# Kernel tuning notes

Measured on AMD Instinct MI355X. Metric: run time of the kernel, lower is better.

Reference implementation:

```python
import jax, jax.numpy as jnp
import numpy as np

B, L, D, K, H = 2, 384, 1024, 128, 32
NUM_EDGES = 25600
NUM_T = 1000
SCALING = K ** -0.5
SQRT_2PI = float(np.sqrt(2.0 * np.pi))


def setup_inputs() -> dict:
    key = jax.random.key(0)
    ks = jax.random.split(key, 20)
    s = 0.02
    inp = {}
    inp["token_id"] = jax.random.randint(ks[0], (B, L), 0, 160)
    inp["is_periodic"] = jnp.zeros((B,), dtype=bool)
    inp["pos"] = 5.0 * jax.random.normal(ks[1], (B, L, 3), dtype=jnp.float32)
    inp["adj"] = jnp.ones((B, L, L), dtype=bool)
    inp["node_type_edge"] = jax.random.randint(ks[2], (B, L, L, 2), 0, NUM_EDGES)
    inp["time_step"] = jax.random.uniform(ks[3], (B, L), dtype=jnp.float32)
    inp["clean_mask"] = jnp.zeros((B, L), dtype=bool)
    # parameters
    inp["embed_w"] = s * jax.random.normal(ks[4], (160, D), dtype=jnp.float32)
    inp["Wpos"] = s * jax.random.normal(ks[5], (K, 3), dtype=jnp.float32)
    inp["Wpfe"] = s * jax.random.normal(ks[6], (D, K), dtype=jnp.float32)
    inp["gbf_means"] = jax.random.normal(ks[7], (K,), dtype=jnp.float32)
    inp["gbf_stds"] = 0.5 + jax.random.uniform(ks[8], (K,), dtype=jnp.float32)
    inp["gbf_mul"] = 1.0 + s * jax.random.normal(ks[9], (NUM_EDGES, 1), dtype=jnp.float32)
    inp["gbf_bias"] = s * jax.random.normal(ks[10], (NUM_EDGES, 1), dtype=jnp.float32)
    inp["W1"] = s * jax.random.normal(ks[11], (K, K), dtype=jnp.float32)
    inp["b1"] = jnp.zeros((K,), dtype=jnp.float32)
    inp["W2"] = s * jax.random.normal(ks[12], (H, K), dtype=jnp.float32)
    inp["b2"] = jnp.zeros((H,), dtype=jnp.float32)
    inp["Wproj"] = s * jax.random.normal(ks[13], (D, K), dtype=jnp.float32)
    inp["bproj"] = jnp.zeros((D,), dtype=jnp.float32)
    inp["Wt1"] = s * jax.random.normal(ks[14], (D, D), dtype=jnp.float32)
    inp["bt1"] = jnp.zeros((D,), dtype=jnp.float32)
    inp["Wt2"] = s * jax.random.normal(ks[15], (D, D), dtype=jnp.float32)
    inp["bt2"] = jnp.zeros((D,), dtype=jnp.float32)
    return inp


def _forward(token_id, is_periodic, pos, adj, node_type_edge, time_step, clean_mask,
             embed_w, Wpos, Wpfe, gbf_means, gbf_stds, gbf_mul, gbf_bias,
             W1, b1, W2, b2, Wproj, bproj, Wt1, bt1, Wt2, bt2):
    padding_mask = token_id == 0                                  # (B,L)
    molecule_mask = (token_id <= 129) & (~is_periodic[:, None])   # (B,L)
    x = embed_w[token_id]                                         # (B,L,D)

    # ---- _pos_emb (non-PBC branch: expand_pos = pos, expand_mask = padding_mask) ----
    delta = pos[:, :, None, :] - pos[:, None, :, :]               # (B,L,L,3)
    dist = jnp.sqrt(jnp.maximum(jnp.sum(delta * delta, -1), 1e-12))  # (B,L,L), safe norm

    # GaussianLayer
    mul = gbf_mul[node_type_edge].sum(-2)                         # (B,L,L,1)
    bias = gbf_bias[node_type_edge].sum(-2)                       # (B,L,L,1)
    y = mul * dist[..., None] + bias                              # (B,L,L,1) -> broadcast K
    std = jnp.abs(gbf_stds) + 1e-5
    a = (y - gbf_means) / std
    edge_feature = jnp.exp(-0.5 * a * a) / (SQRT_2PI * std)       # (B,L,L,K)

    # NonLinear projection to per-head bias
    gab = jax.nn.gelu(edge_feature @ W1.T + b1, approximate=False) @ W2.T + b2  # (B,L,L,H)
    gab = jnp.where(padding_mask[:, None, :, None], -jnp.inf, gab)  # expand-col mask
    gab = jnp.where(padding_mask[:, :, None, None], 0.0, gab)       # padding-row mask
    pos_attn_bias = jnp.transpose(gab, (0, 3, 1, 2))              # (B,H,L,L)

    d = gab.sum(-1)                                               # (B,L,L) sum over heads
    minv = jnp.finfo(jnp.float32).min
    d = jnp.where(padding_mask[:, None, :], minv, d)
    d = jnp.where(padding_mask[:, :, None], minv, d)
    adj_eff = adj | (~molecule_mask[:, :, None])
    d = jnp.where(~adj_eff, minv, d)
    attn = jax.nn.softmax(d * SCALING, axis=-1)                   # (B,L,L)

    pos_e = pos @ Wpos.T                                          # (B,L,K)
    pos_e = jnp.where(padding_mask[..., None], 0.0, pos_e)
    pfe = jnp.einsum('bij,bjk->bik', attn, pos_e)                 # (B,L,K)
    pfe = pfe @ Wpfe.T                                            # (B,L,D)

    ef = jnp.where(padding_mask[:, None, :, None], 0.0, edge_feature).sum(-2)  # (B,L,K)
    pfe = pfe + ef @ Wproj.T + bproj
    pos_embedding = jnp.where(padding_mask[..., None], 0.0, pfe)  # (B,L,D)

    # ---- time step encoder (sinusoidal + MLP) ----
    t = jnp.where(clean_mask, 0.0, time_step) * NUM_T             # (B,L)
    half = D // 2
    freqs = jnp.exp(-jnp.log(10000.0) * jnp.arange(half, dtype=jnp.float32) / half)
    ang = t[..., None] * freqs                                    # (B,L,half)
    sin_emb = jnp.concatenate([jnp.sin(ang), jnp.cos(ang)], -1)   # (B,L,D)
    time_embed = jax.nn.silu(sin_emb @ Wt1.T + bt1) @ Wt2.T + bt2

    x = x + time_embed + pos_embedding
    return x, padding_mask, time_embed, pos_attn_bias, pos_embedding


def reference(token_id, is_periodic, pos, adj, node_type_edge, time_step, clean_mask,
              embed_w, Wpos, Wpfe, gbf_means, gbf_stds, gbf_mul, gbf_bias,
              W1, b1, W2, b2, Wproj, bproj, Wt1, bt1, Wt2, bt2):
    return _forward(token_id, is_periodic, pos, adj, node_type_edge, time_step, clean_mask,
                    embed_w, Wpos, Wpfe, gbf_means, gbf_stds, gbf_mul, gbf_bias,
                    W1, b1, W2, b2, Wproj, bproj, Wt1, bt1, Wt2, bt2)
```

## Files before the change

kernel.cpp:

```cpp
#include <hip/hip_runtime.h>
#include <stddef.h>

#define B_ 2
#define L_ 384
#define D_ 1024
#define K_ 128
#define H_ 32

#define MINV (-3.402823466e38f)
#define NEG_BIG (-1.0e38f)
#define SCALING_ 0.08838834764831845f
#define INV_SQRT_2PI 0.3989422804014327f

typedef __attribute__((ext_vector_type(8))) short bf16x8;
typedef __attribute__((ext_vector_type(4))) float f32x4;

__device__ __forceinline__ float finitize(float x) {
    return fminf(fmaxf(x, -1.0e38f), 1.0e38f);
}
__device__ __forceinline__ unsigned short f2bf(float x) {
    unsigned int u = __float_as_uint(x);
    u += 0x7FFFu + ((u >> 16) & 1u);
    return (unsigned short)(u >> 16);
}
__device__ __forceinline__ unsigned short f2bf_rtz(float x) {
    return (unsigned short)(__float_as_uint(x) >> 16);
}
__device__ __forceinline__ float gelu_tanh(float x) {
    const float x2 = x * x;
    const float z = x * fmaf(0.0356774081f, x2, 0.7978845608f);
    const float e = __expf(2.0f * z);
    const float t = fmaf(-2.0f, __builtin_amdgcn_rcpf(e + 1.0f), 1.0f);
    const float hx = 0.5f * x;
    return fmaf(hx, t, hx);
}

__global__ __launch_bounds__(256) void prep_kernel(
    const float* __restrict__ W1, const float* __restrict__ W2,
    const float* __restrict__ Wpfe, const float* __restrict__ Wproj,
    const float* __restrict__ Wt1, const float* __restrict__ Wt2,
    unsigned short* __restrict__ W1bf, unsigned short* __restrict__ W2bf,
    unsigned short* __restrict__ Wpfebf, unsigned short* __restrict__ Wprojbf,
    unsigned short* __restrict__ Wt1bf, unsigned short* __restrict__ Wt2bf)
{
    const int i = blockIdx.x * 256 + threadIdx.x;
    const float* src; unsigned short* dst; int off;
    if (i < 4096)        { src = W1;    dst = W1bf;    off = i; }
    else if (i < 5120)   { src = W2;    dst = W2bf;    off = i - 4096; }
    else if (i < 37888)  { src = Wpfe;  dst = Wpfebf;  off = i - 5120; }
    else if (i < 70656)  { src = Wproj; dst = Wprojbf; off = i - 37888; }
    else if (i < 332800) { src = Wt1;   dst = Wt1bf;   off = i - 70656; }
    else if (i < 594944) { src = Wt2;   dst = Wt2bf;   off = i - 332800; }
    else return;
    const float4 v = ((const float4*)src)[off];
    ushort4 p; p.x = f2bf(v.x); p.y = f2bf(v.y); p.z = f2bf(v.z); p.w = f2bf(v.w);
    ((ushort4*)dst)[off] = p;
}

__global__ __launch_bounds__(256) void sin_kernel(const float* __restrict__ time_step,
                                                  const unsigned char* __restrict__ clean,
                                                  const int* __restrict__ token,
                                                  unsigned short* __restrict__ sin_bf,
                                                  float* __restrict__ padout)
{
    const int row = blockIdx.x;
    if (threadIdx.x == 0) padout[row] = (token[row] == 0) ? 1.0f : 0.0f;
    const float t = (clean[row] ? 0.0f : time_step[row]) * 1000.0f;
    for (int k = threadIdx.x; k < 512; k += 256) {
        const float f = __expf(-9.210340371976184f * (float)k * (1.0f / 512.0f));
        const float ang = t * f;
        sin_bf[(size_t)row * D_ + k]       = f2bf(__sinf(ang));
        sin_bf[(size_t)row * D_ + 512 + k] = f2bf(__cosf(ang));
    }
}

__global__ __launch_bounds__(256) void gemm_ts(const unsigned short* __restrict__ A,
                                               const unsigned short* __restrict__ Bw,
                                               const float* __restrict__ bias,
                                               void* __restrict__ Cv,
                                               int M, int N, int Kd, int act)
{
    __shared__ unsigned short sA[32][72];
    __shared__ unsigned short sB[64][72];
    const int tid  = threadIdx.x;
    const int lane = tid & 63;
    const int wave = tid >> 6;
    const int l15  = lane & 15;
    const int quad = lane >> 4;
    const int mt   = wave & 1;
    const int np   = wave >> 1;
    const int m0 = blockIdx.y * 32, n0 = blockIdx.x * 64;

    const int ar = tid >> 3,        ac = (tid & 7) * 8;
    const int br0 = tid >> 3,       bc0 = ac;
    const int br1 = (tid + 256) >> 3, bc1 = ac;

    f32x4 acc[2];
#pragma unroll
    for (int t = 0; t < 2; ++t) acc[t] = (f32x4){0.f, 0.f, 0.f, 0.f};

    uint4 ra  = *(const uint4*)&A[(size_t)(m0 + ar) * Kd + ac];
    uint4 rb0 = *(const uint4*)&Bw[(size_t)(n0 + br0) * Kd + bc0];
    uint4 rb1 = *(const uint4*)&Bw[(size_t)(n0 + br1) * Kd + bc1];

    for (int k0 = 0; k0 < Kd; k0 += 64) {
        *(uint4*)&sA[ar][ac]   = ra;
        *(uint4*)&sB[br0][bc0] = rb0;
        *(uint4*)&sB[br1][bc1] = rb1;
        __syncthreads();
        if (k0 + 64 < Kd) {
            ra  = *(const uint4*)&A[(size_t)(m0 + ar) * Kd + k0 + 64 + ac];
            rb0 = *(const uint4*)&Bw[(size_t)(n0 + br0) * Kd + k0 + 64 + bc0];
            rb1 = *(const uint4*)&Bw[(size_t)(n0 + br1) * Kd + k0 + 64 + bc1];
        }
#pragma unroll
        for (int kk = 0; kk < 64; kk += 32) {
            const bf16x8 av = *(const bf16x8*)&sA[mt * 16 + l15][kk + quad * 8];
#pragma unroll
            for (int t = 0; t < 2; ++t) {
                const bf16x8 bv = *(const bf16x8*)&sB[(np * 2 + t) * 16 + l15][kk + quad * 8];
                acc[t] = __builtin_amdgcn_mfma_f32_16x16x32_bf16(av, bv, acc[t], 0, 0, 0);
            }
        }
        __syncthreads();
    }
#pragma unroll
    for (int t = 0; t < 2; ++t) {
        const int nc = n0 + (np * 2 + t) * 16 + l15;
        const float bv = bias[nc];
#pragma unroll
        for (int r = 0; r < 4; ++r) {
            const int mr = m0 + mt * 16 + quad * 4 + r;
            float v = acc[t][r] + bv;
            if (act) {
                v = v / (1.0f + __expf(-v));
                ((unsigned short*)Cv)[(size_t)mr * N + nc] = f2bf(v);
            } else {
                ((float*)Cv)[(size_t)mr * N + nc] = v;
            }
        }
    }
}

__global__ __launch_bounds__(256) void pe_gemm(const unsigned short* __restrict__ pfe_bf,
                                               const unsigned short* __restrict__ ef_bf,
                                               const unsigned short* __restrict__ Wpfebf,
                                               const unsigned short* __restrict__ Wprojbf,
                                               const float* __restrict__ bproj,
                                               const int* __restrict__ token,
                                               const float* __restrict__ embed_w,
                                               const float* __restrict__ te,
                                               float* __restrict__ outPE,
                                               float* __restrict__ outX)
{
    __shared__ unsigned short sA[32][136];
    __shared__ unsigned short sB[64][136];
    const int tid  = threadIdx.x;
    const int lane = tid & 63;
    const int wave = tid >> 6;
    const int l15  = lane & 15;
    const int quad = lane >> 4;
    const int mt   = wave & 1;
    const int np   = wave >> 1;
    const int m0 = blockIdx.y * 32, n0 = blockIdx.x * 64;

    f32x4 acc[2];
#pragma unroll
    for (int t = 0; t < 2; ++t) acc[t] = (f32x4){0.f, 0.f, 0.f, 0.f};

    for (int phase = 0; phase < 2; ++phase) {
        const unsigned short* Ap = phase ? ef_bf : pfe_bf;
        const unsigned short* Bp = phase ? Wprojbf : Wpfebf;
#pragma unroll
        for (int e = tid; e < 512; e += 256) {
            const int r = e >> 4, c8 = (e & 15) * 8;
            *(uint4*)&sA[r][c8] = *(const uint4*)&Ap[(size_t)(m0 + r) * K_ + c8];
        }
#pragma unroll
        for (int e = tid; e < 1024; e += 256) {
            const int r = e >> 4, c8 = (e & 15) * 8;
            *(uint4*)&sB[r][c8] = *(const uint4*)&Bp[(size_t)(n0 + r) * K_ + c8];
        }
        __syncthreads();
#pragma unroll
        for (int ks = 0; ks < 4; ++ks) {
            const bf16x8 av = *(const bf16x8*)&sA[mt * 16 + l15][ks * 32 + quad * 8];
#pragma unroll
            for (int t = 0; t < 2; ++t) {
                const bf16x8 bv = *(const bf16x8*)&sB[(np * 2 + t) * 16 + l15][ks * 32 + quad * 8];
                acc[t] = __builtin_amdgcn_mfma_f32_16x16x32_bf16(av, bv, acc[t], 0, 0, 0);
            }
        }
        __syncthreads();
    }
#pragma unroll
    for (int t = 0; t < 2; ++t) {
        const int nc = n0 + (np * 2 + t) * 16 + l15;
        const float bv = bproj[nc];
#pragma unroll
        for (int r = 0; r < 4; ++r) {
            const int mr = m0 + mt * 16 + quad * 4 + r;
            const int tok = token[mr];
            const float pe = (tok == 0) ? 0.0f : (acc[t][r] + bv);
            outPE[(size_t)mr * D_ + nc] = pe;
            outX[(size_t)mr * D_ + nc] = embed_w[(size_t)tok * D_ + nc]
                                       + te[(size_t)mr * D_ + nc] + pe;
        }
    }
}

__global__ __launch_bounds__(256, 3) void edge_kernel(
    const int* __restrict__ token_id,
    const unsigned char* __restrict__ is_periodic,
    const float* __restrict__ pos,
    const unsigned char* __restrict__ adj,
    const int* __restrict__ nte,
    const float* __restrict__ gbf_means,
    const float* __restrict__ gbf_stds,
    const float* __restrict__ gbf_mul,
    const float* __restrict__ gbf_bias,
    const float* __restrict__ b1,
    const float* __restrict__ b2,
    const float* __restrict__ Wpos,
    const unsigned short* __restrict__ W1bf,
    const unsigned short* __restrict__ W2bf,
    unsigned short* __restrict__ pfe_bf,
    unsigned short* __restrict__ ef_bf,
    float* __restrict__ out_pab)
{
    const int bx = blockIdx.x;
    const int b = bx / L_;
    const int i = bx - b * L_;
    const int row = bx;
    const int tid = threadIdx.x;

    const int tok_i = token_id[row];
    if (tok_i == 0) {
        for (int idx = tid; idx < H_ * L_; idx += 256) {
            const int h = idx / L_;
            const int j = idx - h * L_;
            out_pab[((size_t)(b * H_ + h) * L_ + i) * L_ + j] = 0.0f;
        }
        if (tid < K_) {
            pfe_bf[(size_t)row * K_ + tid] = 0;
            ef_bf[(size_t)row * K_ + tid]  = 0;
        }
        return;
    }

    __shared__ unsigned short sEF[2][32][136];
    __shared__ unsigned short sACT[32][136];
    __shared__ float sGab[32][33];
    __shared__ float sD[L_];
    __shared__ float sRed[256];
    __shared__ float sYall[L_];
    __shared__ unsigned char sPadCol[L_];

    for (int j = tid; j < L_; j += 256)
        sPadCol[j] = (token_id[b * L_ + j] == 0) ? 1 : 0;

    const float px = pos[(size_t)row * 3 + 0];
    const float py = pos[(size_t)row * 3 + 1];
    const float pz = pos[(size_t)row * 3 + 2];
    for (int jg2 = tid; jg2 < L_; jg2 += 256) {
        const float dx = px - pos[(size_t)(b * L_ + jg2) * 3 + 0];
        const float dy = py - pos[(size_t)(b * L_ + jg2) * 3 + 1];
        const float dz = pz - pos[(size_t)(b * L_ + jg2) * 3 + 2];
        const float dist = sqrtf(fmaxf(dx * dx + dy * dy + dz * dz, 1e-12f));
        const size_t eoff = ((size_t)(b * L_ + i) * L_ + jg2) * 2;
        const int e0 = nte[eoff], e1 = nte[eoff + 1];
        sYall[jg2] = (gbf_mul[e0] + gbf_mul[e1]) * dist + (gbf_bias[e0] + gbf_bias[e1]);
    }

    const int lane = tid & 63;
    const int wave = tid >> 6;
    const int l15  = lane & 15;
    const int quad = lane >> 4;
    const int mt   = wave & 1;
    const int ntb  = (wave >> 1) * 4;
    float rb1[4];
#pragma unroll
    for (int nt = 0; nt < 4; ++nt) rb1[nt] = b1[(ntb + nt) * 16 + l15];
    const int hc = (wave >> 1) * 16 + l15;
    const float rb2 = b2[hc];
    bf16x8 w1f[4][4];
#pragma unroll
    for (int ks = 0; ks < 4; ++ks)
#pragma unroll
        for (int nt = 0; nt < 4; ++nt)
            w1f[ks][nt] = *(const bf16x8*)&W1bf[((ntb + nt) * 16 + l15) * K_ + ks * 32 + quad * 8];
    bf16x8 bv2[4];
#pragma unroll
    for (int ks = 0; ks < 4; ++ks)
        bv2[ks] = *(const bf16x8*)&W2bf[hc * K_ + ks * 32 + quad * 8];

    const int kg4 = (tid & 31) * 4;
    const int jg  = tid >> 5;
    const int jb  = jg * 4;
    float meanv[4], istdv[4], cKv[4];
#pragma unroll
    for (int c = 0; c < 4; ++c) {
        meanv[c] = gbf_means[kg4 + c];
        const float s = fabsf(gbf_stds[kg4 + c]) + 1e-5f;
        istdv[c] = 1.0f / s;
        cKv[c]   = INV_SQRT_2PI * istdv[c];
    }
    float efs[4] = {0.f, 0.f, 0.f, 0.f};

    __syncthreads();

#pragma unroll
    for (int jj = 0; jj < 4; ++jj) {
        const int j = jb + jj;
        const float y = sYall[j];
        const bool ok = !sPadCol[j];
        ushort4 p;
#pragma unroll
        for (int c = 0; c < 4; ++c) {
            const float a = (y - meanv[c]) * istdv[c];
            const float ef = __expf(-0.5f * a * a) * cKv[c];
            ((unsigned short*)&p)[c] = f2bf_rtz(ef);
            if (ok) efs[c] += ef;
        }
        *(ushort4*)&sEF[0][j][kg4] = p;
    }
    __syncthreads();

    for (int tile = 0; tile < L_ / 32; ++tile) {
        const int jt0 = tile * 32;
        const int cur = tile & 1, nxt = cur ^ 1;

        f32x4 acc1[4];
#pragma unroll
        for (int nt = 0; nt < 4; ++nt) acc1[nt] = (f32x4){0.f, 0.f, 0.f, 0.f};
#pragma unroll
        for (int ks = 0; ks < 4; ++ks) {
            const bf16x8 av = *(const bf16x8*)&sEF[cur][mt * 16 + l15][ks * 32 + quad * 8];
#pragma unroll
            for (int nt = 0; nt < 4; ++nt)
                acc1[nt] = __builtin_amdgcn_mfma_f32_16x16x32_bf16(av, w1f[ks][nt], acc1[nt], 0, 0, 0);
        }

        if (tile + 1 < L_ / 32) {
            const int jn0 = jt0 + 32;
#pragma unroll
            for (int jj = 0; jj < 4; ++jj) {
                const int j = jb + jj;
                const float y = sYall[jn0 + j];
                const bool ok = !sPadCol[jn0 + j];
                ushort4 p;
#pragma unroll
                for (int c = 0; c < 4; ++c) {
                    const float a = (y - meanv[c]) * istdv[c];
                    const float ef = __expf(-0.5f * a * a) * cKv[c];
                    ((unsigned short*)&p)[c] = f2bf_rtz(ef);
                    if (ok) efs[c] += ef;
                }
                *(ushort4*)&sEF[nxt][j][kg4] = p;
            }
        }

#pragma unroll
        for (int nt = 0; nt < 4; ++nt) {
            const int kkc = (ntb + nt) * 16 + l15;
#pragma unroll
            for (int r = 0; r < 4; ++r) {
                const float v = gelu_tanh(acc1[nt][r] + rb1[nt]);
                sACT[mt * 16 + quad * 4 + r][kkc] = f2bf_rtz(v);
            }
        }
        __syncthreads();

        f32x4 acc2 = (f32x4){0.f, 0.f, 0.f, 0.f};
#pragma unroll
        for (int ks = 0; ks < 4; ++ks) {
            const bf16x8 av = *(const bf16x8*)&sACT[mt * 16 + l15][ks * 32 + quad * 8];
            acc2 = __builtin_amdgcn_mfma_f32_16x16x32_bf16(av, bv2[ks], acc2, 0, 0, 0);
        }
        const int jl0 = mt * 16 + quad * 4;
#pragma unroll
        for (int r = 0; r < 4; ++r) sGab[jl0 + r][hc] = acc2[r] + rb2;
        __syncthreads();

        {
            const int h = tid >> 3, f = tid & 7;
            const int jb2 = f * 4;
            float4 st;
#pragma unroll
            for (int r = 0; r < 4; ++r) {
                float v = finitize(sGab[jb2 + r][h]);
                if (sPadCol[jt0 + jb2 + r]) v = NEG_BIG;
                ((float*)&st)[r] = v;
            }
            *(float4*)&out_pab[((size_t)(b * H_ + h) * L_ + i) * L_ + jt0 + jb2] = st;
        }
        if (tid < 32) {
            float s = 0.0f;
#pragma unroll
            for (int h = 0; h < 32; ++h) s += sGab[tid][h];
            sD[jt0 + tid] = s;
        }
    }

    {
        float* efScr = (float*)sACT;
#pragma unroll
        for (int c = 0; c < 4; ++c) efScr[jg * 128 + kg4 + c] = efs[c];
    }
    __syncthreads();
    if (tid < 128) {
        const float* efScr = (const float*)sACT;
        float s = 0.0f;
#pragma unroll
        for (int g = 0; g < 8; ++g) s += efScr[g * 128 + tid];
        ef_bf[(size_t)row * K_ + tid] = f2bf(s);
    }
    __syncthreads();

    const int lane2 = tid & 63;
    const int wave2 = tid >> 6;
    const bool molecule = (tok_i <= 129) && (is_periodic[b] == 0);
    float lmax = -INFINITY;
    for (int j = tid; j < L_; j += 256) {
        const bool colpad = sPadCol[j] != 0;
        const bool adj_eff = (adj[((size_t)(b * L_ + i)) * L_ + j] != 0) || (!molecule);
        const float dv = (colpad || !adj_eff) ? MINV : sD[j];
        const float s = dv * SCALING_;
        sD[j] = s;
        lmax = fmaxf(lmax, s);
    }
#pragma unroll
    for (int off = 32; off > 0; off >>= 1) lmax = fmaxf(lmax, __shfl_xor(lmax, off));
    if (lane2 == 0) sRed[wave2] = lmax;
    __syncthreads();
    const float smax = fmaxf(fmaxf(sRed[0], sRed[1]), fmaxf(sRed[2], sRed[3]));
    float lsum = 0.0f;
    for (int j = tid; j < L_; j += 256) {
        const float e = __expf(sD[j] - smax);
        sD[j] = e;
        lsum += e;
    }
#pragma unroll
    for (int off = 32; off > 0; off >>= 1) lsum += __shfl_xor(lsum, off);
    if (lane2 == 0) sRed[4 + wave2] = lsum;
    __syncthreads();
    const float inv = 1.0f / (sRed[4] + sRed[5] + sRed[6] + sRed[7]);

    float a0 = 0.f, a1 = 0.f, a2 = 0.f;
    for (int j = tid; j < L_; j += 256) {
        if (!sPadCol[j]) {
            const float e = sD[j];
            a0 += e * pos[(size_t)(b * L_ + j) * 3 + 0];
            a1 += e * pos[(size_t)(b * L_ + j) * 3 + 1];
            a2 += e * pos[(size_t)(b * L_ + j) * 3 + 2];
        }
    }
#pragma unroll
    for (int off = 32; off > 0; off >>= 1) {
        a0 += __shfl_xor(a0, off);
        a1 += __shfl_xor(a1, off);
        a2 += __shfl_xor(a2, off);
    }
    if (lane2 == 0) { sRed[8 + wave2] = a0; sRed[12 + wave2] = a1; sRed[16 + wave2] = a2; }
    __syncthreads();
    if (tid < 128) {
        const float m0 = sRed[8] + sRed[9] + sRed[10] + sRed[11];
        const float m1 = sRed[12] + sRed[13] + sRed[14] + sRed[15];
        const float m2 = sRed[16] + sRed[17] + sRed[18] + sRed[19];
        const float w0 = Wpos[tid * 3 + 0], w1 = Wpos[tid * 3 + 1], w2 = Wpos[tid * 3 + 2];
        pfe_bf[(size_t)row * K_ + tid] = f2bf((m0 * w0 + m1 * w1 + m2 * w2) * inv);
    }
}

extern "C" void kernel_launch(void* const* d_in, const int* in_sizes, int n_in,
                              void* d_out, int out_size, void* d_ws, size_t ws_size,
                              hipStream_t stream) {
    const int*           token_id    = (const int*)d_in[0];
    const unsigned char* is_periodic = (const unsigned char*)d_in[1];
    const float*         pos         = (const float*)d_in[2];
    const unsigned char* adj         = (const unsigned char*)d_in[3];
    const int*           nte         = (const int*)d_in[4];
    const float*         time_step   = (const float*)d_in[5];
    const unsigned char* clean_mask  = (const unsigned char*)d_in[6];
    const float*         embed_w     = (const float*)d_in[7];
    const float*         Wpos        = (const float*)d_in[8];
    const float*         Wpfe        = (const float*)d_in[9];
    const float*         gbf_means   = (const float*)d_in[10];
    const float*         gbf_stds    = (const float*)d_in[11];
    const float*         gbf_mul     = (const float*)d_in[12];
    const float*         gbf_bias    = (const float*)d_in[13];
    const float*         W1          = (const float*)d_in[14];
    const float*         b1          = (const float*)d_in[15];
    const float*         W2          = (const float*)d_in[16];
    const float*         b2          = (const float*)d_in[17];
    const float*         Wproj       = (const float*)d_in[18];
    const float*         bproj       = (const float*)d_in[19];
    const float*         Wt1         = (const float*)d_in[20];
    const float*         bt1         = (const float*)d_in[21];
    const float*         Wt2         = (const float*)d_in[22];
    const float*         bt2         = (const float*)d_in[23];

    float* out = (float*)d_out;
    float* out_x   = out;
    float* out_pad = out + 786432;
    float* out_te  = out + 787200;
    float* out_pab = out + 1573632;
    float* out_pe  = out + 11010816;

    unsigned short* wsu = (unsigned short*)d_ws;
    unsigned short* W1bf    = wsu;
    unsigned short* W2bf    = wsu + 16384;
    unsigned short* Wpfebf  = wsu + 20480;
    unsigned short* Wprojbf = wsu + 151552;
    unsigned short* sin_bf  = wsu + 282624;
    unsigned short* h1_bf   = wsu + 1069056;
    unsigned short* pfe_bf  = wsu + 1855488;
    unsigned short* ef_bf   = wsu + 1953792;
    unsigned short* Wt1bf = (unsigned short*)out_pab;
    unsigned short* Wt2bf = Wt1bf + 1048576;

    prep_kernel<<<dim3(2325), dim3(256), 0, stream>>>(W1, W2, Wpfe, Wproj, Wt1, Wt2,
                                                      W1bf, W2bf, Wpfebf, Wprojbf,
                                                      Wt1bf, Wt2bf);
    sin_kernel<<<dim3(B_ * L_), dim3(256), 0, stream>>>(time_step, clean_mask, token_id,
                                                        sin_bf, out_pad);
    gemm_ts<<<dim3(16, 24), dim3(256), 0, stream>>>(sin_bf, Wt1bf, bt1, (void*)h1_bf,
                                                    768, 1024, 1024, 1);
    gemm_ts<<<dim3(16, 24), dim3(256), 0, stream>>>(h1_bf, Wt2bf, bt2, (void*)out_te,
                                                    768, 1024, 1024, 0);
    edge_kernel<<<dim3(B_ * L_), dim3(256), 0, stream>>>(
        token_id, is_periodic, pos, adj, nte, gbf_means, gbf_stds, gbf_mul, gbf_bias,
        b1, b2, Wpos, W1bf, W2bf, pfe_bf, ef_bf, out_pab);
    pe_gemm<<<dim3(16, 24), dim3(256), 0, stream>>>(pfe_bf, ef_bf, Wpfebf, Wprojbf,
                                                    bproj, token_id, embed_w, out_te,
                                                    out_pe, out_x);
}
```

Baseline: 194.6 us.

## Fuse prep/sin kernels, convert Wt weights in-GEMM, co-schedule edge and first time GEMM

Merges the weight-conversion and sinusoidal-embedding kernels into one launch and drops the separate fp32-to-bf16 conversion of the two large time-MLP weights. The time GEMMs now read fp32 weights and convert them while staging into shared memory. The first time GEMM runs as extra blocks inside the edge kernel's grid, so it overlaps with edge work. The aim is to cut launch count, avoid a full pass over 8 MB of weights, and fill idle CUs during the edge kernel. In exchange, each GEMM block loads twice the weight bytes, and the combined kernel's occupancy is bounded by the edge body's register and shared-memory use.

```diff
diff --git a/kernel.cpp b/kernel.cpp
--- a/kernel.cpp
+++ b/kernel.cpp
@@ -35,53 +35,48 @@
     return fmaf(hx, t, hx);
 }
 
-__global__ __launch_bounds__(256) void prep_kernel(
+__global__ __launch_bounds__(256) void prep_sin_kernel(
     const float* __restrict__ W1, const float* __restrict__ W2,
     const float* __restrict__ Wpfe, const float* __restrict__ Wproj,
-    const float* __restrict__ Wt1, const float* __restrict__ Wt2,
     unsigned short* __restrict__ W1bf, unsigned short* __restrict__ W2bf,
     unsigned short* __restrict__ Wpfebf, unsigned short* __restrict__ Wprojbf,
-    unsigned short* __restrict__ Wt1bf, unsigned short* __restrict__ Wt2bf)
+    const float* __restrict__ time_step, const unsigned char* __restrict__ clean,
+    const int* __restrict__ token, unsigned short* __restrict__ sin_bf,
+    float* __restrict__ padout)
 {
-    const int i = blockIdx.x * 256 + threadIdx.x;
-    const float* src; unsigned short* dst; int off;
-    if (i < 4096)        { src = W1;    dst = W1bf;    off = i; }
-    else if (i < 5120)   { src = W2;    dst = W2bf;    off = i - 4096; }
-    else if (i < 37888)  { src = Wpfe;  dst = Wpfebf;  off = i - 5120; }
-    else if (i < 70656)  { src = Wproj; dst = Wprojbf; off = i - 37888; }
-    else if (i < 332800) { src = Wt1;   dst = Wt1bf;   off = i - 70656; }
-    else if (i < 594944) { src = Wt2;   dst = Wt2bf;   off = i - 332800; }
-    else return;
-    const float4 v = ((const float4*)src)[off];
-    ushort4 p; p.x = f2bf(v.x); p.y = f2bf(v.y); p.z = f2bf(v.z); p.w = f2bf(v.w);
-    ((ushort4*)dst)[off] = p;
-}
-
-__global__ __launch_bounds__(256) void sin_kernel(const float* __restrict__ time_step,
-                                                  const unsigned char* __restrict__ clean,
-                                                  const int* __restrict__ token,
-                                                  unsigned short* __restrict__ sin_bf,
-                                                  float* __restrict__ padout)
+    const int blk = blockIdx.x;
+    if (blk < 276) {
+        const int i = blk * 256 + threadIdx.x;
+        if (i >= 70656) return;
+        const float* src; unsigned short* dst; int off;
+        if (i < 4096)       { src = W1;    dst = W1bf;    off = i; }
+        else if (i < 5120)  { src = W2;    dst = W2bf;    off = i - 4096; }
+        else if (i < 37888) { src = Wpfe;  dst = Wpfebf;  off = i - 5120; }
+        else                { src = Wproj; dst = Wprojbf; off = i - 37888; }
+        const float4 v = ((const float4*)src)[off];
+        ushort4 p; p.x = f2bf(v.x); p.y = f2bf(v.y); p.z = f2bf(v.z); p.w = f2bf(v.w);
+        ((ushort4*)dst)[off] = p;
+    } else {
+        const int row = blk - 276;
+        if (threadIdx.x == 0) padout[row] = (token[row] == 0) ? 1.0f : 0.0f;
+        const float t = (clean[row] ? 0.0f : time_step[row]) * 1000.0f;
+        for (int k = threadIdx.x; k < 512; k += 256) {
+            const float f = __expf(-9.210340371976184f * (float)k * (1.0f / 512.0f));
+            const float ang = t * f;
+            sin_bf[(size_t)row * D_ + k]       = f2bf(__sinf(ang));
+            sin_bf[(size_t)row * D_ + 512 + k] = f2bf(__cosf(ang));
+        }
+    }
+}
+
+__device__ __forceinline__ void gemm_ts_body(
+    char* smem, int m0, int n0,
+    const unsigned short* __restrict__ A, const float* __restrict__ Bw,
+    const float* __restrict__ bias, void* __restrict__ Cv,
+    int N, int Kd, int act)
 {
-    const int row = blockIdx.x;
-    if (threadIdx.x == 0) padout[row] = (token[row] == 0) ? 1.0f : 0.0f;
-    const float t = (clean[row] ? 0.0f : time_step[row]) * 1000.0f;
-    for (int k = threadIdx.x; k < 512; k += 256) {
-        const float f = __expf(-9.210340371976184f * (float)k * (1.0f / 512.0f));
-        const float ang = t * f;
-        sin_bf[(size_t)row * D_ + k]       = f2bf(__sinf(ang));
-        sin_bf[(size_t)row * D_ + 512 + k] = f2bf(__cosf(ang));
-    }
-}
-
-__global__ __launch_bounds__(256) void gemm_ts(const unsigned short* __restrict__ A,
-                                               const unsigned short* __restrict__ Bw,
-                                               const float* __restrict__ bias,
-                                               void* __restrict__ Cv,
-                                               int M, int N, int Kd, int act)
-{
-    __shared__ unsigned short sA[32][72];
-    __shared__ unsigned short sB[64][72];
+    unsigned short (*sA)[72] = (unsigned short(*)[72])smem;
+    unsigned short (*sB)[72] = (unsigned short(*)[72])(smem + 4608);
     const int tid  = threadIdx.x;
     const int lane = tid & 63;
     const int wave = tid >> 6;
@@ -89,29 +84,35 @@
     const int quad = lane >> 4;
     const int mt   = wave & 1;
     const int np   = wave >> 1;
-    const int m0 = blockIdx.y * 32, n0 = blockIdx.x * 64;
-
-    const int ar = tid >> 3,        ac = (tid & 7) * 8;
-    const int br0 = tid >> 3,       bc0 = ac;
-    const int br1 = (tid + 256) >> 3, bc1 = ac;
+
+    const int ar = tid >> 3, ac = (tid & 7) * 8;
+    const int bc4 = (tid & 15) * 4;
 
     f32x4 acc[2];
 #pragma unroll
     for (int t = 0; t < 2; ++t) acc[t] = (f32x4){0.f, 0.f, 0.f, 0.f};
 
-    uint4 ra  = *(const uint4*)&A[(size_t)(m0 + ar) * Kd + ac];
-    uint4 rb0 = *(const uint4*)&Bw[(size_t)(n0 + br0) * Kd + bc0];
-    uint4 rb1 = *(const uint4*)&Bw[(size_t)(n0 + br1) * Kd + bc1];
+    uint4 ra = *(const uint4*)&A[(size_t)(m0 + ar) * Kd + ac];
+    float4 rbv[4];
+#pragma unroll
+    for (int c = 0; c < 4; ++c)
+        rbv[c] = *(const float4*)&Bw[(size_t)(n0 + ((tid + c * 256) >> 4)) * Kd + bc4];
 
     for (int k0 = 0; k0 < Kd; k0 += 64) {
-        *(uint4*)&sA[ar][ac]   = ra;
-        *(uint4*)&sB[br0][bc0] = rb0;
-        *(uint4*)&sB[br1][bc1] = rb1;
+        *(uint4*)&sA[ar][ac] = ra;
+#pragma unroll
+        for (int c = 0; c < 4; ++c) {
+            ushort4 p;
+            p.x = f2bf(rbv[c].x); p.y = f2bf(rbv[c].y);
+            p.z = f2bf(rbv[c].z); p.w = f2bf(rbv[c].w);
+            *(ushort4*)&sB[(tid + c * 256) >> 4][bc4] = p;
+        }
         __syncthreads();
         if (k0 + 64 < Kd) {
-            ra  = *(const uint4*)&A[(size_t)(m0 + ar) * Kd + k0 + 64 + ac];
-            rb0 = *(const uint4*)&Bw[(size_t)(n0 + br0) * Kd + k0 + 64 + bc0];
-            rb1 = *(const uint4*)&Bw[(size_t)(n0 + br1) * Kd + k0 + 64 + bc1];
+            ra = *(const uint4*)&A[(size_t)(m0 + ar) * Kd + k0 + 64 + ac];
+#pragma unroll
+            for (int c = 0; c < 4; ++c)
+                rbv[c] = *(const float4*)&Bw[(size_t)(n0 + ((tid + c * 256) >> 4)) * Kd + k0 + 64 + bc4];
         }
 #pragma unroll
         for (int kk = 0; kk < 64; kk += 32) {
@@ -140,6 +141,314 @@
             }
         }
     }
+}
+
+__device__ __forceinline__ void edge_body(
+    char* smem, int row,
+    const int* __restrict__ token_id,
+    const unsigned char* __restrict__ is_periodic,
+    const float* __restrict__ pos,
+    const unsigned char* __restrict__ adj,
+    const int* __restrict__ nte,
+    const float* __restrict__ gbf_means,
+    const float* __restrict__ gbf_stds,
+    const float* __restrict__ gbf_mul,
+    const float* __restrict__ gbf_bias,
+    const float* __restrict__ b1,
+    const float* __restrict__ b2,
+    const float* __restrict__ Wpos,
+    const unsigned short* __restrict__ W1bf,
+    const unsigned short* __restrict__ W2bf,
+    unsigned short* __restrict__ pfe_bf,
+    unsigned short* __restrict__ ef_bf,
+    float* __restrict__ out_pab)
+{
+    const int b = row / L_;
+    const int i = row - b * L_;
+    const int tid = threadIdx.x;
+
+    const int tok_i = token_id[row];
+    if (tok_i == 0) {
+        for (int idx = tid; idx < H_ * L_; idx += 256) {
+            const int h = idx / L_;
+            const int j = idx - h * L_;
+            out_pab[((size_t)(b * H_ + h) * L_ + i) * L_ + j] = 0.0f;
+        }
+        if (tid < K_) {
+            pfe_bf[(size_t)row * K_ + tid] = 0;
+            ef_bf[(size_t)row * K_ + tid]  = 0;
+        }
+        return;
+    }
+
+    typedef unsigned short efbuf_t[32][136];
+    efbuf_t* sEF = (efbuf_t*)smem;
+    unsigned short (*sACT)[136] = (unsigned short(*)[136])(smem + 17408);
+    float (*sGab)[33] = (float(*)[33])(smem + 26112);
+    float* sD      = (float*)(smem + 30336);
+    float* sRed    = (float*)(smem + 31872);
+    float* sYall   = (float*)(smem + 32896);
+    unsigned char* sPadCol = (unsigned char*)(smem + 34432);
+
+    for (int j = tid; j < L_; j += 256)
+        sPadCol[j] = (token_id[b * L_ + j] == 0) ? 1 : 0;
+
+    const float px = pos[(size_t)row * 3 + 0];
+    const float py = pos[(size_t)row * 3 + 1];
+    const float pz = pos[(size_t)row * 3 + 2];
+    for (int jg2 = tid; jg2 < L_; jg2 += 256) {
+        const float dx = px - pos[(size_t)(b * L_ + jg2) * 3 + 0];
+        const float dy = py - pos[(size_t)(b * L_ + jg2) * 3 + 1];
+        const float dz = pz - pos[(size_t)(b * L_ + jg2) * 3 + 2];
+        const float dist = sqrtf(fmaxf(dx * dx + dy * dy + dz * dz, 1e-12f));
+        const size_t eoff = ((size_t)(b * L_ + i) * L_ + jg2) * 2;
+        const int e0 = nte[eoff], e1 = nte[eoff + 1];
+        sYall[jg2] = (gbf_mul[e0] + gbf_mul[e1]) * dist + (gbf_bias[e0] + gbf_bias[e1]);
+    }
+
+    const int lane = tid & 63;
+    const int wave = tid >> 6;
+    const int l15  = lane & 15;
+    const int quad = lane >> 4;
+    const int mt   = wave & 1;
+    const int ntb  = (wave >> 1) * 4;
+    float rb1[4];
+#pragma unroll
+    for (int nt = 0; nt < 4; ++nt) rb1[nt] = b1[(ntb + nt) * 16 + l15];
+    const int hc = (wave >> 1) * 16 + l15;
+    const float rb2 = b2[hc];
+    bf16x8 w1f[4][4];
+#pragma unroll
+    for (int ks = 0; ks < 4; ++ks)
+#pragma unroll
+        for (int nt = 0; nt < 4; ++nt)
+            w1f[ks][nt] = *(const bf16x8*)&W1bf[((ntb + nt) * 16 + l15) * K_ + ks * 32 + quad * 8];
+    bf16x8 bv2[4];
+#pragma unroll
+    for (int ks = 0; ks < 4; ++ks)
+        bv2[ks] = *(const bf16x8*)&W2bf[hc * K_ + ks * 32 + quad * 8];
+
+    const int kg4 = (tid & 31) * 4;
+    const int jg  = tid >> 5;
+    const int jb  = jg * 4;
+    float meanv[4], istdv[4], cKv[4];
+#pragma unroll
+    for (int c = 0; c < 4; ++c) {
+        meanv[c] = gbf_means[kg4 + c];
+        const float s = fabsf(gbf_stds[kg4 + c]) + 1e-5f;
+        istdv[c] = 1.0f / s;
+        cKv[c]   = INV_SQRT_2PI * istdv[c];
+    }
+    float efs[4] = {0.f, 0.f, 0.f, 0.f};
+
+    __syncthreads();
+
+#pragma unroll
+    for (int jj = 0; jj < 4; ++jj) {
+        const int j = jb + jj;
+        const float y = sYall[j];
+        const bool ok = !sPadCol[j];
+        ushort4 p;
+#pragma unroll
+        for (int c = 0; c < 4; ++c) {
+            const float a = (y - meanv[c]) * istdv[c];
+            const float ef = __expf(-0.5f * a * a) * cKv[c];
+            ((unsigned short*)&p)[c] = f2bf_rtz(ef);
+            if (ok) efs[c] += ef;
+        }
+        *(ushort4*)&sEF[0][j][kg4] = p;
+    }
+    __syncthreads();
+
+    for (int tile = 0; tile < L_ / 32; ++tile) {
+        const int jt0 = tile * 32;
+        const int cur = tile & 1, nxt = cur ^ 1;
+
+        f32x4 acc1[4];
+#pragma unroll
+        for (int nt = 0; nt < 4; ++nt) acc1[nt] = (f32x4){0.f, 0.f, 0.f, 0.f};
+#pragma unroll
+        for (int ks = 0; ks < 4; ++ks) {
+            const bf16x8 av = *(const bf16x8*)&sEF[cur][mt * 16 + l15][ks * 32 + quad * 8];
+#pragma unroll
+            for (int nt = 0; nt < 4; ++nt)
+                acc1[nt] = __builtin_amdgcn_mfma_f32_16x16x32_bf16(av, w1f[ks][nt], acc1[nt], 0, 0, 0);
+        }
+
+        if (tile + 1 < L_ / 32) {
+            const int jn0 = jt0 + 32;
+#pragma unroll
+            for (int jj = 0; jj < 4; ++jj) {
+                const int j = jb + jj;
+                const float y = sYall[jn0 + j];
+                const bool ok = !sPadCol[jn0 + j];
+                ushort4 p;
+#pragma unroll
+                for (int c = 0; c < 4; ++c) {
+                    const float a = (y - meanv[c]) * istdv[c];
+                    const float ef = __expf(-0.5f * a * a) * cKv[c];
+                    ((unsigned short*)&p)[c] = f2bf_rtz(ef);
+                    if (ok) efs[c] += ef;
+                }
+                *(ushort4*)&sEF[nxt][j][kg4] = p;
+            }
+        }
+
+#pragma unroll
+        for (int nt = 0; nt < 4; ++nt) {
+            const int kkc = (ntb + nt) * 16 + l15;
+#pragma unroll
+            for (int r = 0; r < 4; ++r) {
+                const float v = gelu_tanh(acc1[nt][r] + rb1[nt]);
+                sACT[mt * 16 + quad * 4 + r][kkc] = f2bf_rtz(v);
+            }
+        }
+        __syncthreads();
+
+        f32x4 acc2 = (f32x4){0.f, 0.f, 0.f, 0.f};
+#pragma unroll
+        for (int ks = 0; ks < 4; ++ks) {
+            const bf16x8 av = *(const bf16x8*)&sACT[mt * 16 + l15][ks * 32 + quad * 8];
+            acc2 = __builtin_amdgcn_mfma_f32_16x16x32_bf16(av, bv2[ks], acc2, 0, 0, 0);
+        }
+        const int jl0 = mt * 16 + quad * 4;
+#pragma unroll
+        for (int r = 0; r < 4; ++r) sGab[jl0 + r][hc] = acc2[r] + rb2;
+        __syncthreads();
+
+        {
+            const int h = tid >> 3, f = tid & 7;
+            const int jb2 = f * 4;
+            float4 st;
+#pragma unroll
+            for (int r = 0; r < 4; ++r) {
+                float v = finitize(sGab[jb2 + r][h]);
+                if (sPadCol[jt0 + jb2 + r]) v = NEG_BIG;
+                ((float*)&st)[r] = v;
+            }
+            *(float4*)&out_pab[((size_t)(b * H_ + h) * L_ + i) * L_ + jt0 + jb2] = st;
+        }
+        if (tid < 32) {
+            float s = 0.0f;
+#pragma unroll
+            for (int h = 0; h < 32; ++h) s += sGab[tid][h];
+            sD[jt0 + tid] = s;
+        }
+    }
+
+    {
+        float* efScr = (float*)sACT;
+#pragma unroll
+        for (int c = 0; c < 4; ++c) efScr[jg * 128 + kg4 + c] = efs[c];
+    }
+    __syncthreads();
+    if (tid < 128) {
+        const float* efScr = (const float*)sACT;
+        float s = 0.0f;
+#pragma unroll
+        for (int g = 0; g < 8; ++g) s += efScr[g * 128 + tid];
+        ef_bf[(size_t)row * K_ + tid] = f2bf(s);
+    }
+    __syncthreads();
+
+    const bool molecule = (tok_i <= 129) && (is_periodic[b] == 0);
+    float lmax = -INFINITY;
+    for (int j = tid; j < L_; j += 256) {
+        const bool colpad = sPadCol[j] != 0;
+        const bool adj_eff = (adj[((size_t)(b * L_ + i)) * L_ + j] != 0) || (!molecule);
+        const float dv = (colpad || !adj_eff) ? MINV : sD[j];
+        const float s = dv * SCALING_;
+        sD[j] = s;
+        lmax = fmaxf(lmax, s);
+    }
+#pragma unroll
+    for (int off = 32; off > 0; off >>= 1) lmax = fmaxf(lmax, __shfl_xor(lmax, off));
+    if (lane == 0) sRed[wave] = lmax;
+    __syncthreads();
+    const float smax = fmaxf(fmaxf(sRed[0], sRed[1]), fmaxf(sRed[2], sRed[3]));
+    float lsum = 0.0f;
+    for (int j = tid; j < L_; j += 256) {
+        const float e = __expf(sD[j] - smax);
+        sD[j] = e;
+        lsum += e;
+    }
+#pragma unroll
+    for (int off = 32; off > 0; off >>= 1) lsum += __shfl_xor(lsum, off);
+    if (lane == 0) sRed[4 + wave] = lsum;
+    __syncthreads();
+    const float inv = 1.0f / (sRed[4] + sRed[5] + sRed[6] + sRed[7]);
+
+    float a0 = 0.f, a1 = 0.f, a2 = 0.f;
+    for (int j = tid; j < L_; j += 256) {
+        if (!sPadCol[j]) {
+            const float e = sD[j];
+            a0 += e * pos[(size_t)(b * L_ + j) * 3 + 0];
+            a1 += e * pos[(size_t)(b * L_ + j) * 3 + 1];
+            a2 += e * pos[(size_t)(b * L_ + j) * 3 + 2];
+        }
+    }
+#pragma unroll
+    for (int off = 32; off > 0; off >>= 1) {
+        a0 += __shfl_xor(a0, off);
+        a1 += __shfl_xor(a1, off);
+        a2 += __shfl_xor(a2, off);
+    }
+    if (lane == 0) { sRed[8 + wave] = a0; sRed[12 + wave] = a1; sRed[16 + wave] = a2; }
+    __syncthreads();
+    if (tid < 128) {
+        const float m0 = sRed[8] + sRed[9] + sRed[10] + sRed[11];
+        const float m1 = sRed[12] + sRed[13] + sRed[14] + sRed[15];
+        const float m2 = sRed[16] + sRed[17] + sRed[18] + sRed[19];
+        const float w0 = Wpos[tid * 3 + 0], w1 = Wpos[tid * 3 + 1], w2 = Wpos[tid * 3 + 2];
+        pfe_bf[(size_t)row * K_ + tid] = f2bf((m0 * w0 + m1 * w1 + m2 * w2) * inv);
+    }
+}
+
+__global__ __launch_bounds__(256, 3) void edge_ts1(
+    const int* __restrict__ token_id,
+    const unsigned char* __restrict__ is_periodic,
+    const float* __restrict__ pos,
+    const unsigned char* __restrict__ adj,
+    const int* __restrict__ nte,
+    const float* __restrict__ gbf_means,
+    const float* __restrict__ gbf_stds,
+    const float* __restrict__ gbf_mul,
+    const float* __restrict__ gbf_bias,
+    const float* __restrict__ b1,
+    const float* __restrict__ b2,
+    const float* __restrict__ Wpos,
+    const unsigned short* __restrict__ W1bf,
+    const unsigned short* __restrict__ W2bf,
+    unsigned short* __restrict__ pfe_bf,
+    unsigned short* __restrict__ ef_bf,
+    float* __restrict__ out_pab,
+    const unsigned short* __restrict__ sin_bf,
+    const float* __restrict__ Wt1,
+    const float* __restrict__ bt1,
+    unsigned short* __restrict__ h1_bf)
+{
+    __shared__ __align__(16) char smem[34816];
+    const int bx = blockIdx.x;
+    if (bx < B_ * L_) {
+        edge_body(smem, bx, token_id, is_periodic, pos, adj, nte,
+                  gbf_means, gbf_stds, gbf_mul, gbf_bias, b1, b2, Wpos,
+                  W1bf, W2bf, pfe_bf, ef_bf, out_pab);
+    } else {
+        const int tsb = bx - B_ * L_;
+        const int m0 = (tsb >> 4) * 32;
+        const int n0 = (tsb & 15) * 64;
+        gemm_ts_body(smem, m0, n0, sin_bf, Wt1, bt1, (void*)h1_bf, D_, D_, 1);
+    }
+}
+
+__global__ __launch_bounds__(256) void gemm_ts2(const unsigned short* __restrict__ A,
+                                                const float* __restrict__ Bw,
+                                                const float* __restrict__ bias,
+                                                float* __restrict__ C)
+{
+    __shared__ __align__(16) char smem[13824];
+    gemm_ts_body(smem, blockIdx.y * 32, blockIdx.x * 64, A, Bw, bias, (void*)C,
+                 D_, D_, 0);
 }
 
 __global__ __launch_bounds__(256) void pe_gemm(const unsigned short* __restrict__ pfe_bf,
@@ -206,269 +515,6 @@
             outX[(size_t)mr * D_ + nc] = embed_w[(size_t)tok * D_ + nc]
                                        + te[(size_t)mr * D_ + nc] + pe;
         }
-    }
-}
-
-__global__ __launch_bounds__(256, 3) void edge_kernel(
-    const int* __restrict__ token_id,
-    const unsigned char* __restrict__ is_periodic,
-    const float* __restrict__ pos,
-    const unsigned char* __restrict__ adj,
-    const int* __restrict__ nte,
-    const float* __restrict__ gbf_means,
-    const float* __restrict__ gbf_stds,
-    const float* __restrict__ gbf_mul,
-    const float* __restrict__ gbf_bias,
-    const float* __restrict__ b1,
-    const float* __restrict__ b2,
-    const float* __restrict__ Wpos,
-    const unsigned short* __restrict__ W1bf,
-    const unsigned short* __restrict__ W2bf,
-    unsigned short* __restrict__ pfe_bf,
-    unsigned short* __restrict__ ef_bf,
-    float* __restrict__ out_pab)
-{
-    const int bx = blockIdx.x;
-    const int b = bx / L_;
-    const int i = bx - b * L_;
-    const int row = bx;
-    const int tid = threadIdx.x;
-
-    const int tok_i = token_id[row];
-    if (tok_i == 0) {
-        for (int idx = tid; idx < H_ * L_; idx += 256) {
-            const int h = idx / L_;
-            const int j = idx - h * L_;
-            out_pab[((size_t)(b * H_ + h) * L_ + i) * L_ + j] = 0.0f;
-        }
-        if (tid < K_) {
-            pfe_bf[(size_t)row * K_ + tid] = 0;
-            ef_bf[(size_t)row * K_ + tid]  = 0;
-        }
-        return;
-    }
-
-    __shared__ unsigned short sEF[2][32][136];
-    __shared__ unsigned short sACT[32][136];
-    __shared__ float sGab[32][33];
-    __shared__ float sD[L_];
-    __shared__ float sRed[256];
-    __shared__ float sYall[L_];
-    __shared__ unsigned char sPadCol[L_];
-
-    for (int j = tid; j < L_; j += 256)
-        sPadCol[j] = (token_id[b * L_ + j] == 0) ? 1 : 0;
-
-    const float px = pos[(size_t)row * 3 + 0];
-    const float py = pos[(size_t)row * 3 + 1];
-    const float pz = pos[(size_t)row * 3 + 2];
-    for (int jg2 = tid; jg2 < L_; jg2 += 256) {
-        const float dx = px - pos[(size_t)(b * L_ + jg2) * 3 + 0];
-        const float dy = py - pos[(size_t)(b * L_ + jg2) * 3 + 1];
-        const float dz = pz - pos[(size_t)(b * L_ + jg2) * 3 + 2];
-        const float dist = sqrtf(fmaxf(dx * dx + dy * dy + dz * dz, 1e-12f));
-        const size_t eoff = ((size_t)(b * L_ + i) * L_ + jg2) * 2;
-        const int e0 = nte[eoff], e1 = nte[eoff + 1];
-        sYall[jg2] = (gbf_mul[e0] + gbf_mul[e1]) * dist + (gbf_bias[e0] + gbf_bias[e1]);
-    }
-
-    const int lane = tid & 63;
-    const int wave = tid >> 6;
-    const int l15  = lane & 15;
-    const int quad = lane >> 4;
-    const int mt   = wave & 1;
-    const int ntb  = (wave >> 1) * 4;
-    float rb1[4];
-#pragma unroll
-    for (int nt = 0; nt < 4; ++nt) rb1[nt] = b1[(ntb + nt) * 16 + l15];
-    const int hc = (wave >> 1) * 16 + l15;
-    const float rb2 = b2[hc];
-    bf16x8 w1f[4][4];
-#pragma unroll
-    for (int ks = 0; ks < 4; ++ks)
-#pragma unroll
-        for (int nt = 0; nt < 4; ++nt)
-            w1f[ks][nt] = *(const bf16x8*)&W1bf[((ntb + nt) * 16 + l15) * K_ + ks * 32 + quad * 8];
-    bf16x8 bv2[4];
-#pragma unroll
-    for (int ks = 0; ks < 4; ++ks)
-        bv2[ks] = *(const bf16x8*)&W2bf[hc * K_ + ks * 32 + quad * 8];
-
-    const int kg4 = (tid & 31) * 4;
-    const int jg  = tid >> 5;
-    const int jb  = jg * 4;
-    float meanv[4], istdv[4], cKv[4];
-#pragma unroll
-    for (int c = 0; c < 4; ++c) {
-        meanv[c] = gbf_means[kg4 + c];
-        const float s = fabsf(gbf_stds[kg4 + c]) + 1e-5f;
-        istdv[c] = 1.0f / s;
-        cKv[c]   = INV_SQRT_2PI * istdv[c];
-    }
-    float efs[4] = {0.f, 0.f, 0.f, 0.f};
-
-    __syncthreads();
-
-#pragma unroll
-    for (int jj = 0; jj < 4; ++jj) {
-        const int j = jb + jj;
-        const float y = sYall[j];
-        const bool ok = !sPadCol[j];
-        ushort4 p;
-#pragma unroll
-        for (int c = 0; c < 4; ++c) {
-            const float a = (y - meanv[c]) * istdv[c];
-            const float ef = __expf(-0.5f * a * a) * cKv[c];
-            ((unsigned short*)&p)[c] = f2bf_rtz(ef);
-            if (ok) efs[c] += ef;
-        }
-        *(ushort4*)&sEF[0][j][kg4] = p;
-    }
-    __syncthreads();
-
-    for (int tile = 0; tile < L_ / 32; ++tile) {
-        const int jt0 = tile * 32;
-        const int cur = tile & 1, nxt = cur ^ 1;
-
-        f32x4 acc1[4];
-#pragma unroll
-        for (int nt = 0; nt < 4; ++nt) acc1[nt] = (f32x4){0.f, 0.f, 0.f, 0.f};
-#pragma unroll
-        for (int ks = 0; ks < 4; ++ks) {
-            const bf16x8 av = *(const bf16x8*)&sEF[cur][mt * 16 + l15][ks * 32 + quad * 8];
-#pragma unroll
-            for (int nt = 0; nt < 4; ++nt)
-                acc1[nt] = __builtin_amdgcn_mfma_f32_16x16x32_bf16(av, w1f[ks][nt], acc1[nt], 0, 0, 0);
-        }
-
-        if (tile + 1 < L_ / 32) {
-            const int jn0 = jt0 + 32;
-#pragma unroll
-            for (int jj = 0; jj < 4; ++jj) {
-                const int j = jb + jj;
-                const float y = sYall[jn0 + j];
-                const bool ok = !sPadCol[jn0 + j];
-                ushort4 p;
-#pragma unroll
-                for (int c = 0; c < 4; ++c) {
-                    const float a = (y - meanv[c]) * istdv[c];
-                    const float ef = __expf(-0.5f * a * a) * cKv[c];
-                    ((unsigned short*)&p)[c] = f2bf_rtz(ef);
-                    if (ok) efs[c] += ef;
-                }
-                *(ushort4*)&sEF[nxt][j][kg4] = p;
-            }
-        }
-
-#pragma unroll
-        for (int nt = 0; nt < 4; ++nt) {
-            const int kkc = (ntb + nt) * 16 + l15;
-#pragma unroll
-            for (int r = 0; r < 4; ++r) {
-                const float v = gelu_tanh(acc1[nt][r] + rb1[nt]);
-                sACT[mt * 16 + quad * 4 + r][kkc] = f2bf_rtz(v);
-            }
-        }
-        __syncthreads();
-
-        f32x4 acc2 = (f32x4){0.f, 0.f, 0.f, 0.f};
-#pragma unroll
-        for (int ks = 0; ks < 4; ++ks) {
-            const bf16x8 av = *(const bf16x8*)&sACT[mt * 16 + l15][ks * 32 + quad * 8];
-            acc2 = __builtin_amdgcn_mfma_f32_16x16x32_bf16(av, bv2[ks], acc2, 0, 0, 0);
-        }
-        const int jl0 = mt * 16 + quad * 4;
-#pragma unroll
-        for (int r = 0; r < 4; ++r) sGab[jl0 + r][hc] = acc2[r] + rb2;
-        __syncthreads();
-
-        {
-            const int h = tid >> 3, f = tid & 7;
-            const int jb2 = f * 4;
-            float4 st;
-#pragma unroll
-            for (int r = 0; r < 4; ++r) {
-                float v = finitize(sGab[jb2 + r][h]);
-                if (sPadCol[jt0 + jb2 + r]) v = NEG_BIG;
-                ((float*)&st)[r] = v;
-            }
-            *(float4*)&out_pab[((size_t)(b * H_ + h) * L_ + i) * L_ + jt0 + jb2] = st;
-        }
-        if (tid < 32) {
-            float s = 0.0f;
-#pragma unroll
-            for (int h = 0; h < 32; ++h) s += sGab[tid][h];
-            sD[jt0 + tid] = s;
-        }
-    }
-
-    {
-        float* efScr = (float*)sACT;
-#pragma unroll
-        for (int c = 0; c < 4; ++c) efScr[jg * 128 + kg4 + c] = efs[c];
-    }
-    __syncthreads();
-    if (tid < 128) {
-        const float* efScr = (const float*)sACT;
-        float s = 0.0f;
-#pragma unroll
-        for (int g = 0; g < 8; ++g) s += efScr[g * 128 + tid];
-        ef_bf[(size_t)row * K_ + tid] = f2bf(s);
-    }
-    __syncthreads();
-
-    const int lane2 = tid & 63;
-    const int wave2 = tid >> 6;
-    const bool molecule = (tok_i <= 129) && (is_periodic[b] == 0);
-    float lmax = -INFINITY;
-    for (int j = tid; j < L_; j += 256) {
-        const bool colpad = sPadCol[j] != 0;
-        const bool adj_eff = (adj[((size_t)(b * L_ + i)) * L_ + j] != 0) || (!molecule);
-        const float dv = (colpad || !adj_eff) ? MINV : sD[j];
-        const float s = dv * SCALING_;
-        sD[j] = s;
-        lmax = fmaxf(lmax, s);
-    }
-#pragma unroll
-    for (int off = 32; off > 0; off >>= 1) lmax = fmaxf(lmax, __shfl_xor(lmax, off));
-    if (lane2 == 0) sRed[wave2] = lmax;
-    __syncthreads();
-    const float smax = fmaxf(fmaxf(sRed[0], sRed[1]), fmaxf(sRed[2], sRed[3]));
-    float lsum = 0.0f;
-    for (int j = tid; j < L_; j += 256) {
-        const float e = __expf(sD[j] - smax);
-        sD[j] = e;
-        lsum += e;
-    }
-#pragma unroll
-    for (int off = 32; off > 0; off >>= 1) lsum += __shfl_xor(lsum, off);
-    if (lane2 == 0) sRed[4 + wave2] = lsum;
-    __syncthreads();
-    const float inv = 1.0f / (sRed[4] + sRed[5] + sRed[6] + sRed[7]);
-
-    float a0 = 0.f, a1 = 0.f, a2 = 0.f;
-    for (int j = tid; j < L_; j += 256) {
-        if (!sPadCol[j]) {
-            const float e = sD[j];
-            a0 += e * pos[(size_t)(b * L_ + j) * 3 + 0];
-            a1 += e * pos[(size_t)(b * L_ + j) * 3 + 1];
-            a2 += e * pos[(size_t)(b * L_ + j) * 3 + 2];
-        }
-    }
-#pragma unroll
-    for (int off = 32; off > 0; off >>= 1) {
-        a0 += __shfl_xor(a0, off);
-        a1 += __shfl_xor(a1, off);
-        a2 += __shfl_xor(a2, off);
-    }
-    if (lane2 == 0) { sRed[8 + wave2] = a0; sRed[12 + wave2] = a1; sRed[16 + wave2] = a2; }
-    __syncthreads();
-    if (tid < 128) {
-        const float m0 = sRed[8] + sRed[9] + sRed[10] + sRed[11];
-        const float m1 = sRed[12] + sRed[13] + sRed[14] + sRed[15];
-        const float m2 = sRed[16] + sRed[17] + sRed[18] + sRed[19];
-        const float w0 = Wpos[tid * 3 + 0], w1 = Wpos[tid * 3 + 1], w2 = Wpos[tid * 3 + 2];
-        pfe_bf[(size_t)row * K_ + tid] = f2bf((m0 * w0 + m1 * w1 + m2 * w2) * inv);
     }
 }
 
@@ -516,21 +562,15 @@
     unsigned short* h1_bf   = wsu + 1069056;
     unsigned short* pfe_bf  = wsu + 1855488;
     unsigned short* ef_bf   = wsu + 1953792;
-    unsigned short* Wt1bf = (unsigned short*)out_pab;
-    unsigned short* Wt2bf = Wt1bf + 1048576;
-
-    prep_kernel<<<dim3(2325), dim3(256), 0, stream>>>(W1, W2, Wpfe, Wproj, Wt1, Wt2,
-                                                      W1bf, W2bf, Wpfebf, Wprojbf,
-                                                      Wt1bf, Wt2bf);
-    sin_kernel<<<dim3(B_ * L_), dim3(256), 0, stream>>>(time_step, clean_mask, token_id,
-                                                        sin_bf, out_pad);
-    gemm_ts<<<dim3(16, 24), dim3(256), 0, stream>>>(sin_bf, Wt1bf, bt1, (void*)h1_bf,
-                                                    768, 1024, 1024, 1);
-    gemm_ts<<<dim3(16, 24), dim3(256), 0, stream>>>(h1_bf, Wt2bf, bt2, (void*)out_te,
-                                                    768, 1024, 1024, 0);
-    edge_kernel<<<dim3(B_ * L_), dim3(256), 0, stream>>>(
+
+    prep_sin_kernel<<<dim3(1044), dim3(256), 0, stream>>>(
+        W1, W2, Wpfe, Wproj, W1bf, W2bf, Wpfebf, Wprojbf,
+        time_step, clean_mask, token_id, sin_bf, out_pad);
+    edge_ts1<<<dim3(B_ * L_ + 384), dim3(256), 0, stream>>>(
         token_id, is_periodic, pos, adj, nte, gbf_means, gbf_stds, gbf_mul, gbf_bias,
-        b1, b2, Wpos, W1bf, W2bf, pfe_bf, ef_bf, out_pab);
+        b1, b2, Wpos, W1bf, W2bf, pfe_bf, ef_bf, out_pab,
+        sin_bf, Wt1, bt1, h1_bf);
+    gemm_ts2<<<dim3(16, 24), dim3(256), 0, stream>>>(h1_bf, Wt2, bt2, out_te);
     pe_gemm<<<dim3(16, 24), dim3(256), 0, stream>>>(pfe_bf, ef_bf, Wpfebf, Wprojbf,
                                                     bproj, token_id, embed_w, out_te,
                                                     out_pe, out_x);
```

Measured after the change: 190.6 us. -2.1%, faster.
